# Kernel optimization log

Measured on AMD Instinct MI355X. Metric: run time of the kernel, lower is better.

## Reference

```python
import jax, jax.numpy as jnp
import numpy as np

IMAGE_SIZE = 512
VOXEL_SIZE = 0.7  # mm per voxel; distances are rescaled to voxel units (vox_scaling = 1/VOXEL_SIZE)
CHUNK = 64        # angles processed per scan step in backprojection


def _ramp_rfft(det):
    """Kak-Slaney spatial-domain ram-lak kernel -> rfft filter (scikit/torch_radon style)."""
    size = max(64, 2 ** int(np.ceil(np.log2(2 * det))))
    n = np.concatenate([np.arange(1, size // 2 + 1, 2), np.arange(size // 2 - 1, 0, -2)])
    f = np.zeros(size, np.float64)
    f[0] = 0.25
    f[1::2] = -1.0 / (np.pi * n) ** 2
    filt = 2.0 * np.real(np.fft.fft(f))[: size // 2 + 1]
    return jnp.asarray(filt.astype(np.float32)), size


def _filter_sinogram(sino, det):
    # sino: [A, det]; ramp filter along detector axis with zero-padding to pow2
    filt, size = _ramp_rfft(det)
    s = jnp.pad(sino, ((0, 0), (0, size - det)))
    F = jnp.fft.rfft(s, axis=-1) * filt
    return jnp.fft.irfft(F, n=size, axis=-1)[:, :det]


def _backproject(q, betas, dso_s, du_v, N, det):
    # q: [A, det] filtered sinogram, betas: [A] source angles.
    xs = jnp.arange(N, dtype=jnp.float32) - (N - 1) / 2.0
    X = xs[None, :]   # image columns -> x
    Y = xs[:, None]   # image rows    -> y
    center = (det - 1) / 2.0
    A = q.shape[0]
    nc = A // CHUNK
    gather = jax.vmap(lambda row, idx: row[idx])  # per-angle detector gather

    def body(acc, inp):
        b, qc = inp  # b: [CHUNK], qc: [CHUNK, det]
        sin = jnp.sin(b)[:, None, None]
        cos = jnp.cos(b)[:, None, None]
        # source at (-dso*sin(b), dso*cos(b)); U = distance of pixel projected on source->iso axis
        U = dso_s + X * sin - Y * cos                       # [CHUNK, N, N]
        u = dso_s * (X * cos + Y * sin) / (U * du_v) + center  # virtual-detector index
        i0f = jnp.floor(u)
        w = u - i0f
        i0 = i0f.astype(jnp.int32)
        q0 = gather(qc, jnp.clip(i0, 0, det - 1))
        q1 = gather(qc, jnp.clip(i0 + 1, 0, det - 1))
        valid = (u >= 0.0) & (u <= det - 1.0)
        contrib = jnp.where(valid, (q0 * (1.0 - w) + q1 * w) * (dso_s / U) ** 2, 0.0)
        return acc + contrib.sum(0), None

    acc, _ = jax.lax.scan(jax.checkpoint(body),
                          jnp.zeros((N, N), jnp.float32),
                          (betas.reshape(nc, CHUNK), q.reshape(nc, CHUNK, det)))
    return acc


def _reconstruct_single(sino, angles_hr, dso, ddo, du, hu):
    # sino: [A_sr, det]; angles_hr: [A_hr] (only start + increment used, as in torch code)
    vox = 1.0 / VOXEL_SIZE
    A_sr, det = sino.shape
    A_hr = angles_hr.shape[0]
    sino = sino * vox
    dso_s = vox * dso
    sd_s = vox * (dso + ddo)  # source-to-detector
    du_s = vox * du
    du_v = du_s * dso_s / sd_s  # detector spacing rescaled to virtual detector at isocenter
    # super-resolved angle grid: linspace(start, start + A_hr*inc, A_sr, endpoint=False)
    inc = angles_hr[1] - angles_hr[0]
    dbeta = (A_hr * inc) / A_sr
    betas = angles_hr[0] + dbeta * jnp.arange(A_sr, dtype=jnp.float32)
    # fan-beam cosine pre-weighting on virtual detector
    uk = (jnp.arange(det, dtype=jnp.float32) - (det - 1) / 2.0) * du_v
    cosw = dso_s / jnp.sqrt(dso_s ** 2 + uk ** 2)
    filtered = _filter_sinogram(sino * cosw, det) / du_v
    reco = _backproject(filtered, betas, dso_s, du_v, IMAGE_SIZE, det) * (0.5 * dbeta)
    hu0 = jnp.maximum(jnp.abs(hu), 1e-6)
    return 1000.0 * (reco - hu0) / (hu0 + 1e-6)


def setup_inputs() -> dict:
    key = jax.random.key(0)
    B, A_HR, A_SR, DET = 2, 1152, 1152, 736
    sinogram = jax.random.normal(key, (B, 1, A_SR, DET), jnp.float32)
    angles = jnp.tile(jnp.linspace(0.0, 2.0 * np.pi, A_HR, endpoint=False,
                                   dtype=jnp.float32)[None], (B, 1))
    dso = jnp.full((B,), 595.0, jnp.float32)     # source-to-isocenter [mm]
    ddo = jnp.full((B,), 490.6, jnp.float32)     # isocenter-to-detector [mm]
    du = jnp.full((B,), 1.2858, jnp.float32)     # detector pixel pitch [mm]
    hu_factor = jnp.full((B,), 0.02, jnp.float32)
    return {"sinogram": sinogram, "angles": angles, "dso": dso, "ddo": ddo,
            "du": du, "hu_factor": hu_factor}


def reference(sinogram, angles, dso, ddo, du, hu_factor):
    # batch loop in torch -> vmap here (per-sample geometry)
    reco = jax.vmap(_reconstruct_single)(sinogram[:, 0], angles, dso, ddo, du, hu_factor)
    return reco[:, None].astype(jnp.float32)  # (B, 1, N, N)
```

## Files before the change

kernel.cpp:

```cpp
#include <hip/hip_runtime.h>
#include <math.h>

#define PB_SIZE 3056
#define W_OFF   2304
#define S_OFF   3040

__global__ void prep_kernel(const float* __restrict__ angles,
                            const float* __restrict__ dso,
                            const float* __restrict__ ddo,
                            const float* __restrict__ du,
                            const float* __restrict__ hu,
                            float* __restrict__ ws, int nang, int ndet, int B)
{
    int b = blockIdx.x;
    int t = threadIdx.x;
    const float vox = 1.0f / 0.7f;
    float dsov = dso[b];
    float dso_s = vox * dsov;
    float sd_s  = vox * (dsov + ddo[b]);
    float du_s  = vox * du[b];
    float du_v  = du_s * dso_s / sd_s;
    float beta0 = angles[(size_t)b * nang];
    float dbeta = angles[(size_t)b * nang + 1] - beta0;
    float center = 0.5f * (float)(ndet - 1);

    for (int d = t; d < ndet; d += blockDim.x) {
        float v = 0.0f;
        if (d == 0) v = 0.5f;
        else if (d & 1) {
            float pd = 3.14159265358979323846f * (float)d;
            v = -2.0f / (pd * pd);
        }
        ws[d] = v;
    }

    float* pb = ws + 736 + b * PB_SIZE;
    for (int i = t; i < nang; i += blockDim.x) {
        float beta = beta0 + dbeta * (float)i;
        pb[2 * i]     = sinf(beta);
        pb[2 * i + 1] = cosf(beta);
    }
    float* w = pb + W_OFF;
    for (int j = t; j < ndet; j += blockDim.x) {
        float uk = ((float)j - center) * du_v;
        float cosw = dso_s / sqrtf(dso_s * dso_s + uk * uk);
        w[j] = vox * cosw / du_v;
    }
    if (t == 0) {
        float hu0 = fabsf(hu[b]);
        if (hu0 < 1e-6f) hu0 = 1e-6f;
        float* s = pb + S_OFF;
        s[0] = dso_s;
        s[1] = dso_s / du_v;
        s[2] = center;
        s[3] = 1000.0f * 0.5f * dbeta / (hu0 + 1e-6f);
        s[4] = -1000.0f * hu0 / (hu0 + 1e-6f);
        if (b == 0) {
            int same = 0;
            if (B == 2) {
                same = (dso[0] == dso[1]) && (ddo[0] == ddo[1]) && (du[0] == du[1]) &&
                       (angles[0] == angles[nang]) && (angles[1] == angles[nang + 1]);
            }
            s[5] = (float)same;
        }
    }
}

__global__ __launch_bounds__(256) void filter_kernel(const float* __restrict__ sino,
                                                     const float* __restrict__ ws,
                                                     float* __restrict__ filtered,
                                                     int nang, int ndet)
{
    __shared__ float row[3 * 736];
    __shared__ float hl[736];
    int a = blockIdx.x;
    int b = blockIdx.y;
    int t = threadIdx.x;
    const float* srow = sino + ((size_t)b * nang + a) * (size_t)ndet;
    const float* wtab = ws + 736 + b * PB_SIZE + W_OFF;

    for (int i = t; i < 736; i += 256) {
        row[i] = 0.0f;
        row[1472 + i] = 0.0f;
    }
    for (int j = t; j < ndet; j += 256)
        row[736 + j] = srow[j] * wtab[j];
    for (int d = t; d < 736; d += 256)
        hl[d] = ws[d];
    __syncthreads();

    float* frow = filtered + ((size_t)b * nang + a) * (size_t)ndet;
    for (int i = t; i < ndet; i += 256) {
        const float* rp = row + 736 + i;
        float acc = 0.5f * rp[0];
        #pragma unroll 4
        for (int d = 1; d < 736; d += 2) {
            acc += hl[d] * (rp[-d] + rp[d]);
        }
        frow[i] = acc;
    }
}

__global__ __launch_bounds__(256) void backproject_fused(const float* __restrict__ ws,
                                                         const float* __restrict__ filtered,
                                                         float* __restrict__ out,
                                                         int nang, int ndet, int B)
{
    __shared__ float sc[2 * 1152];
    int tid = threadIdx.y * 16 + threadIdx.x;
    int cx = blockIdx.x * 16 + threadIdx.x;
    int cy = blockIdx.y * 16 + threadIdx.y;
    float X = (float)cx - 255.5f;
    float Y = (float)cy - 255.5f;

    const float* pb0 = ws + 736;
    const float* sp0 = pb0 + S_OFF;
    int fused = (sp0[5] != 0.0f);

    if (fused) {
        for (int i = tid; i < 2 * nang; i += 256)
            sc[i] = pb0[i];
        __syncthreads();
        float dso_s = sp0[0];
        float k1    = sp0[1];
        float hc    = sp0[2];
        const float* sp1 = sp0 + PB_SIZE;
        float Xk = X * k1;
        float Yk = Y * k1;
        const float* fb0 = filtered;
        const float* fb1 = filtered + (size_t)nang * ndet;
        float acc0 = 0.0f, acc1 = 0.0f;
        int rowoff = 0;
        for (int a = 0; a < nang; ++a, rowoff += ndet) {
            float s = sc[2 * a];
            float c = sc[2 * a + 1];
            float U = fmaf(X, s, dso_s) - Y * c;
            float r = __builtin_amdgcn_rcpf(U);
            float ts = fmaf(Xk, c, Yk * s);
            float v  = ts * r;
            float u  = v + hc;
            float fi = floorf(u);
            float w  = u - fi;
            int i0   = (int)fi;
            int i0c  = min(max(i0, 0), ndet - 1);
            int i1c  = min(i0c + 1, ndet - 1);
            float d  = dso_s * r;
            float wt = d * d;
            wt = (fabsf(v) <= hc) ? wt : 0.0f;
            float q00 = fb0[rowoff + i0c];
            float q01 = fb0[rowoff + i1c];
            float q10 = fb1[rowoff + i0c];
            float q11 = fb1[rowoff + i1c];
            acc0 = fmaf(fmaf(q01 - q00, w, q00), wt, acc0);
            acc1 = fmaf(fmaf(q11 - q10, w, q10), wt, acc1);
        }
        size_t px = (size_t)cy * 512 + cx;
        out[px]              = fmaf(sp0[3], acc0, sp0[4]);
        out[px + 512 * 512]  = fmaf(sp1[3], acc1, sp1[4]);
    } else {
        for (int b = 0; b < B; ++b) {
            const float* pb = ws + 736 + b * PB_SIZE;
            const float* sp = pb + S_OFF;
            __syncthreads();
            for (int i = tid; i < 2 * nang; i += 256)
                sc[i] = pb[i];
            __syncthreads();
            float dso_s = sp[0];
            float k1    = sp[1];
            float center= sp[2];
            float As    = sp[3];
            float Bs    = sp[4];
            const float* fb = filtered + (size_t)b * nang * ndet;
            float acc = 0.0f;
            float detm1 = (float)(ndet - 1);
            for (int a = 0; a < nang; ++a) {
                float s = sc[2 * a];
                float c = sc[2 * a + 1];
                float U = dso_s + X * s - Y * c;
                float r = __builtin_amdgcn_rcpf(U);
                float t = X * c + Y * s;
                float u = k1 * t * r + center;
                float fi = floorf(u);
                float w = u - fi;
                int i0 = (int)fi;
                int i0c = min(max(i0, 0), ndet - 1);
                int i1c = min(max(i0 + 1, 0), ndet - 1);
                const float* frow = fb + (size_t)a * ndet;
                float q0 = frow[i0c];
                float q1 = frow[i1c];
                float d = dso_s * r;
                float wt = d * d;
                bool valid = (u >= 0.0f) && (u <= detm1);
                float val = q0 + (q1 - q0) * w;
                acc += valid ? val * wt : 0.0f;
            }
            out[((size_t)b * 512 + cy) * 512 + cx] = As * acc + Bs;
        }
    }
}

extern "C" void kernel_launch(void* const* d_in, const int* in_sizes, int n_in,
                              void* d_out, int out_size, void* d_ws, size_t ws_size,
                              hipStream_t stream)
{
    const float* sino   = (const float*)d_in[0];
    const float* angles = (const float*)d_in[1];
    const float* dso    = (const float*)d_in[2];
    const float* ddo    = (const float*)d_in[3];
    const float* du     = (const float*)d_in[4];
    const float* hu     = (const float*)d_in[5];
    float* ws  = (float*)d_ws;
    float* out = (float*)d_out;

    int B    = in_sizes[2];
    int nang = in_sizes[1] / B;
    int ndet = in_sizes[0] / (B * nang);

    float* filtered = ws + 736 + B * PB_SIZE;

    prep_kernel<<<B, 256, 0, stream>>>(angles, dso, ddo, du, hu, ws, nang, ndet, B);
    filter_kernel<<<dim3(nang, B), 256, 0, stream>>>(sino, ws, filtered, nang, ndet);
    backproject_fused<<<dim3(512 / 16, 512 / 16), dim3(16, 16), 0, stream>>>(
        ws, filtered, out, nang, ndet, B);
}
```

Measured before the change: 498.3 us.

## Split backprojection over angle halves and store interleaved detector pairs

The filter kernel now writes each filtered sample together with its right neighbour as a float2, so backprojection does one 8-byte gather per sinogram instead of two scalar gathers. Backprojection splits the angle loop across two z-slices of the grid to double the block count from 1024. Partial sums go to a workspace buffer and a new combine kernel adds them and applies the HU scaling. This costs twice the filtered-data memory, an extra partial-buffer round trip and one more launch.

```diff
diff --git a/kernel.cpp b/kernel.cpp
--- a/kernel.cpp
+++ b/kernel.cpp
@@ -4,6 +4,7 @@
 #define PB_SIZE 3056
 #define W_OFF   2304
 #define S_OFF   3040
+#define NSPLIT  2
 
 __global__ void prep_kernel(const float* __restrict__ angles,
                             const float* __restrict__ dso,
@@ -68,11 +69,12 @@
 
 __global__ __launch_bounds__(256) void filter_kernel(const float* __restrict__ sino,
                                                      const float* __restrict__ ws,
-                                                     float* __restrict__ filtered,
+                                                     float2* __restrict__ pairs,
                                                      int nang, int ndet)
 {
     __shared__ float row[3 * 736];
     __shared__ float hl[736];
+    __shared__ float fout[744];
     int a = blockIdx.x;
     int b = blockIdx.y;
     int t = threadIdx.x;
@@ -89,7 +91,6 @@
         hl[d] = ws[d];
     __syncthreads();
 
-    float* frow = filtered + ((size_t)b * nang + a) * (size_t)ndet;
     for (int i = t; i < ndet; i += 256) {
         const float* rp = row + 736 + i;
         float acc = 0.5f * rp[0];
@@ -97,41 +98,55 @@
         for (int d = 1; d < 736; d += 2) {
             acc += hl[d] * (rp[-d] + rp[d]);
         }
-        frow[i] = acc;
-    }
+        fout[i] = acc;
+    }
+    __syncthreads();
+    if (t == 0) fout[ndet] = fout[ndet - 1];
+    __syncthreads();
+
+    float2* prow = pairs + ((size_t)b * nang + a) * (size_t)ndet;
+    for (int j = t; j < ndet; j += 256)
+        prow[j] = make_float2(fout[j], fout[j + 1]);
 }
 
 __global__ __launch_bounds__(256) void backproject_fused(const float* __restrict__ ws,
-                                                         const float* __restrict__ filtered,
-                                                         float* __restrict__ out,
+                                                         const float2* __restrict__ pairs,
+                                                         float* __restrict__ partial,
                                                          int nang, int ndet, int B)
 {
-    __shared__ float sc[2 * 1152];
+    __shared__ float sc[2304];
     int tid = threadIdx.y * 16 + threadIdx.x;
     int cx = blockIdx.x * 16 + threadIdx.x;
     int cy = blockIdx.y * 16 + threadIdx.y;
+    int z  = blockIdx.z;
     float X = (float)cx - 255.5f;
     float Y = (float)cy - 255.5f;
+
+    int na_s = (nang + NSPLIT - 1) / NSPLIT;
+    int a0 = z * na_s;
+    int a1 = min(nang, a0 + na_s);
+    int nas = a1 - a0;
 
     const float* pb0 = ws + 736;
     const float* sp0 = pb0 + S_OFF;
     int fused = (sp0[5] != 0.0f);
+    int px = cy * 512 + cx;
 
     if (fused) {
-        for (int i = tid; i < 2 * nang; i += 256)
-            sc[i] = pb0[i];
+        for (int i = tid; i < 2 * nas; i += 256)
+            sc[i] = pb0[2 * a0 + i];
         __syncthreads();
         float dso_s = sp0[0];
         float k1    = sp0[1];
         float hc    = sp0[2];
-        const float* sp1 = sp0 + PB_SIZE;
         float Xk = X * k1;
         float Yk = Y * k1;
-        const float* fb0 = filtered;
-        const float* fb1 = filtered + (size_t)nang * ndet;
+        const float2* pr0 = pairs + (size_t)a0 * ndet;
+        const float2* pr1 = pairs + (size_t)(nang + a0) * ndet;
         float acc0 = 0.0f, acc1 = 0.0f;
         int rowoff = 0;
-        for (int a = 0; a < nang; ++a, rowoff += ndet) {
+        #pragma unroll 2
+        for (int a = 0; a < nas; ++a, rowoff += ndet) {
             float s = sc[2 * a];
             float c = sc[2 * a + 1];
             float U = fmaf(X, s, dso_s) - Y * c;
@@ -143,60 +158,66 @@
             float w  = u - fi;
             int i0   = (int)fi;
             int i0c  = min(max(i0, 0), ndet - 1);
-            int i1c  = min(i0c + 1, ndet - 1);
+            float2 p0 = pr0[rowoff + i0c];
+            float2 p1 = pr1[rowoff + i0c];
             float d  = dso_s * r;
             float wt = d * d;
             wt = (fabsf(v) <= hc) ? wt : 0.0f;
-            float q00 = fb0[rowoff + i0c];
-            float q01 = fb0[rowoff + i1c];
-            float q10 = fb1[rowoff + i0c];
-            float q11 = fb1[rowoff + i1c];
-            acc0 = fmaf(fmaf(q01 - q00, w, q00), wt, acc0);
-            acc1 = fmaf(fmaf(q11 - q10, w, q10), wt, acc1);
-        }
-        size_t px = (size_t)cy * 512 + cx;
-        out[px]              = fmaf(sp0[3], acc0, sp0[4]);
-        out[px + 512 * 512]  = fmaf(sp1[3], acc1, sp1[4]);
+            acc0 = fmaf(fmaf(p0.y - p0.x, w, p0.x), wt, acc0);
+            acc1 = fmaf(fmaf(p1.y - p1.x, w, p1.x), wt, acc1);
+        }
+        partial[(size_t)(z * B + 0) * 262144 + px] = acc0;
+        partial[(size_t)(z * B + 1) * 262144 + px] = acc1;
     } else {
         for (int b = 0; b < B; ++b) {
             const float* pb = ws + 736 + b * PB_SIZE;
             const float* sp = pb + S_OFF;
             __syncthreads();
-            for (int i = tid; i < 2 * nang; i += 256)
-                sc[i] = pb[i];
+            for (int i = tid; i < 2 * nas; i += 256)
+                sc[i] = pb[2 * a0 + i];
             __syncthreads();
             float dso_s = sp[0];
             float k1    = sp[1];
-            float center= sp[2];
-            float As    = sp[3];
-            float Bs    = sp[4];
-            const float* fb = filtered + (size_t)b * nang * ndet;
+            float hc    = sp[2];
+            const float2* pr = pairs + (size_t)(b * nang + a0) * ndet;
             float acc = 0.0f;
-            float detm1 = (float)(ndet - 1);
-            for (int a = 0; a < nang; ++a) {
+            int rowoff = 0;
+            for (int a = 0; a < nas; ++a, rowoff += ndet) {
                 float s = sc[2 * a];
                 float c = sc[2 * a + 1];
-                float U = dso_s + X * s - Y * c;
+                float U = fmaf(X, s, dso_s) - Y * c;
                 float r = __builtin_amdgcn_rcpf(U);
-                float t = X * c + Y * s;
-                float u = k1 * t * r + center;
+                float ts = k1 * fmaf(X, c, Y * s);
+                float v  = ts * r;
+                float u  = v + hc;
                 float fi = floorf(u);
-                float w = u - fi;
-                int i0 = (int)fi;
-                int i0c = min(max(i0, 0), ndet - 1);
-                int i1c = min(max(i0 + 1, 0), ndet - 1);
-                const float* frow = fb + (size_t)a * ndet;
-                float q0 = frow[i0c];
-                float q1 = frow[i1c];
-                float d = dso_s * r;
+                float w  = u - fi;
+                int i0   = (int)fi;
+                int i0c  = min(max(i0, 0), ndet - 1);
+                float2 p = pr[rowoff + i0c];
+                float d  = dso_s * r;
                 float wt = d * d;
-                bool valid = (u >= 0.0f) && (u <= detm1);
-                float val = q0 + (q1 - q0) * w;
-                acc += valid ? val * wt : 0.0f;
+                wt = (fabsf(v) <= hc) ? wt : 0.0f;
+                acc = fmaf(fmaf(p.y - p.x, w, p.x), wt, acc);
             }
-            out[((size_t)b * 512 + cy) * 512 + cx] = As * acc + Bs;
-        }
-    }
+            partial[(size_t)(z * B + b) * 262144 + px] = acc;
+        }
+    }
+}
+
+__global__ __launch_bounds__(256) void combine_kernel(const float* __restrict__ partial,
+                                                      const float* __restrict__ ws,
+                                                      float* __restrict__ out, int B)
+{
+    int idx = blockIdx.x * 256 + threadIdx.x;
+    int bb = idx >> 18;
+    int px = idx & 262143;
+    const float* sp = ws + 736 + bb * PB_SIZE + S_OFF;
+    float v = 0.0f;
+    #pragma unroll
+    for (int z = 0; z < NSPLIT; ++z)
+        v += partial[(size_t)(z * B + bb) * 262144 + px];
+    out[idx] = fmaf(sp[3], v, sp[4]);
 }
 
 extern "C" void kernel_launch(void* const* d_in, const int* in_sizes, int n_in,
@@ -216,10 +237,12 @@
     int nang = in_sizes[1] / B;
     int ndet = in_sizes[0] / (B * nang);
 
-    float* filtered = ws + 736 + B * PB_SIZE;
+    float2* pairs   = (float2*)(ws + 736 + B * PB_SIZE);
+    float*  partial = ws + 736 + B * PB_SIZE + (size_t)B * nang * ndet * 2;
 
     prep_kernel<<<B, 256, 0, stream>>>(angles, dso, ddo, du, hu, ws, nang, ndet, B);
-    filter_kernel<<<dim3(nang, B), 256, 0, stream>>>(sino, ws, filtered, nang, ndet);
-    backproject_fused<<<dim3(512 / 16, 512 / 16), dim3(16, 16), 0, stream>>>(
-        ws, filtered, out, nang, ndet, B);
-}
+    filter_kernel<<<dim3(nang, B), 256, 0, stream>>>(sino, ws, pairs, nang, ndet);
+    backproject_fused<<<dim3(32, 32, NSPLIT), dim3(16, 16), 0, stream>>>(
+        ws, pairs, partial, nang, ndet, B);
+    combine_kernel<<<(B * 262144) / 256, 256, 0, stream>>>(partial, ws, out, B);
+}
```

Measured after the change: 565.6 us. 13.5% more time.
